# Performance work log

Measured on AMD Instinct MI355X. Metric: run time of the kernel, lower is better.

The kernel has to match this reference:

```python
import jax, jax.numpy as jnp
import numpy as np
import math

N_NODES = 20000
N_EDGES = 320000
DIM = 256
NUM_HEADS = 8


def setup_inputs() -> dict:
    key = jax.random.key(0)
    ks = jax.random.split(key, 8)
    x = jax.random.normal(ks[0], (N_NODES, DIM), dtype=jnp.float32)
    edge_index = jax.random.randint(ks[1], (2, N_EDGES), 0, N_NODES, dtype=jnp.int64)
    edge_attr = jax.random.normal(ks[2], (N_EDGES, DIM), dtype=jnp.float32)
    s = 1.0 / math.sqrt(DIM)
    Wq = jax.random.uniform(ks[3], (DIM, DIM), jnp.float32, -s, s)
    Wk = jax.random.uniform(ks[4], (DIM, DIM), jnp.float32, -s, s)
    Wv = jax.random.uniform(ks[5], (DIM, DIM), jnp.float32, -s, s)
    We = jax.random.uniform(ks[6], (DIM, DIM), jnp.float32, -s, s)
    be = jax.random.uniform(ks[7], (DIM,), jnp.float32, -s, s)
    return {"x": x, "edge_index": edge_index, "edge_attr": edge_attr,
            "Wq": Wq, "Wk": Wk, "Wv": Wv, "We": We, "be": be}


def reference(x, edge_index, edge_attr, Wq, Wk, Wv, We, be):
    N = x.shape[0]
    E = edge_attr.shape[0]
    H = NUM_HEADS
    C = DIM // H  # per-head channels (concat=True)
    src = edge_index[0]  # segment / attention-grouping index
    dst = edge_index[1]
    # Z = edge_attr * x[dst]  -> [E, D]
    Z = edge_attr * x[dst]
    q = x @ Wq.T          # [N, D]
    k = Z @ Wk.T          # [E, D]
    v = Z @ Wv.T          # [E, D]
    edge_out = Z @ We.T + be  # [E, D]
    # split heads
    qh = q.reshape(N, H, C)
    kh = k.reshape(E, H, C)
    vh = v.reshape(E, H, C)
    # per-edge, per-head score: sum(q[src]*k)/sqrt(C)   -> [E, H]
    scores = jnp.einsum('ehc,ehc->eh', qh[src], kh) / math.sqrt(C)
    # segment softmax grouped by src node
    m = jax.ops.segment_max(scores, src, num_segments=N)        # [N, H]
    ex = jnp.exp(scores - m[src])                               # [E, H]
    denom = jax.ops.segment_sum(ex, src, num_segments=N)        # [N, H]
    attn = ex / (denom[src] + 1e-16)                            # [E, H]
    # weighted scatter-sum of values -> [N, H, C] -> [N, D]
    out = jax.ops.segment_sum(attn[:, :, None] * vh, src, num_segments=N)
    out = out.reshape(N, H * C)
    return (out, edge_out)
```

## Files before the change

kernel.cpp:

```cpp
#include <hip/hip_runtime.h>
#include <math.h>

#define NN 20000
#define NE 320000
#define DIM 256

typedef __bf16 bf16x8 __attribute__((ext_vector_type(8)));
typedef float f32x4 __attribute__((ext_vector_type(4)));
typedef int i32x4 __attribute__((ext_vector_type(4)));
typedef unsigned short u16x4 __attribute__((ext_vector_type(4)));

union B8 { i32x4 i; bf16x8 b; };

__device__ __forceinline__ unsigned short f2bf(float f) {
  unsigned int u; __builtin_memcpy(&u, &f, 4);
  u += 0x7fffu + ((u >> 16) & 1u);
  return (unsigned short)(u >> 16);
}
__device__ __forceinline__ float bf2f(unsigned short h) {
  unsigned int u = ((unsigned int)h) << 16;
  float f; __builtin_memcpy(&f, &u, 4);
  return f;
}

#define GLOAD16(gp, lp)                                                        \
  __builtin_amdgcn_global_load_lds(                                            \
      (const __attribute__((address_space(1))) unsigned int*)(gp),             \
      (__attribute__((address_space(3))) unsigned int*)(lp), 16, 0, 0)

__global__ __launch_bounds__(256) void pack_w(const float* __restrict__ W,
                                              unsigned short* __restrict__ wf) {
  int t = blockIdx.x * 256 + threadIdx.x;
  int lane = t & 63, ct = (t >> 6) & 15, ks = t >> 10;
  int col = ct * 16 + (lane & 15);
  int k0 = ks * 32 + (lane >> 4) * 8;
  const float* src = W + col * 256 + k0;
  unsigned int h[8];
#pragma unroll
  for (int j = 0; j < 8; j++) h[j] = f2bf(src[j]);
  i32x4 v;
  v.x = (int)(h[0] | (h[1] << 16));
  v.y = (int)(h[2] | (h[3] << 16));
  v.z = (int)(h[4] | (h[5] << 16));
  v.w = (int)(h[6] | (h[7] << 16));
  ((i32x4*)wf)[t] = v;
}

__global__ __launch_bounds__(256) void zprep(const float* __restrict__ x,
                                             const int* __restrict__ ei,
                                             const float* __restrict__ ea,
                                             unsigned short* __restrict__ zg) {
  int idx = blockIdx.x * 256 + threadIdx.x;
  int lane = idx & 63;
  int bt = (idx >> 6) & 3;
  int ks = (idx >> 8) & 7;
  int tile = idx >> 11;
  int e = tile * 64 + bt * 16 + (lane & 15);
  int kf = ks * 32 + (lane >> 4) * 8;
  int dst = ei[NE + e];
  const f32x4* ap = (const f32x4*)(ea + (size_t)e * DIM + kf);
  const f32x4* xp = (const f32x4*)(x + (size_t)dst * DIM + kf);
  f32x4 p0 = ap[0] * xp[0];
  f32x4 p1 = ap[1] * xp[1];
  unsigned int h[8];
  h[0] = f2bf(p0.x); h[1] = f2bf(p0.y); h[2] = f2bf(p0.z); h[3] = f2bf(p0.w);
  h[4] = f2bf(p1.x); h[5] = f2bf(p1.y); h[6] = f2bf(p1.z); h[7] = f2bf(p1.w);
  i32x4 o;
  o.x = (int)(h[0] | (h[1] << 16));
  o.y = (int)(h[2] | (h[3] << 16));
  o.z = (int)(h[4] | (h[5] << 16));
  o.w = (int)(h[6] | (h[7] << 16));
  size_t byteo = (size_t)tile * 65536 + (size_t)(idx & 2047) * 16;
  *(i32x4*)((char*)zg + byteo) = o;
}

__device__ __forceinline__ void gemm_tile(const unsigned short* zs,
                                          const unsigned short* wf,
                                          int lane, int wv, f32x4 (&acc)[4][4]) {
#pragma unroll 1
  for (int ksI = 0; ksI < 8; ksI++) {
    bf16x8 afr[4], bfr[4];
#pragma unroll
    for (int rt = 0; rt < 4; rt++) {
      int row = rt * 16 + (lane & 15);
      int k = ksI * 32 + (lane >> 4) * 8;
      int byteo = (row * 512 + k * 2) ^ ((row & 7) << 4);
      B8 u; u.i = *(const i32x4*)((const char*)zs + byteo);
      afr[rt] = u.b;
    }
#pragma unroll
    for (int ct = 0; ct < 4; ct++) {
      B8 u; u.i = ((const i32x4*)wf)[ksI * 1024 + (wv * 4 + ct) * 64 + lane];
      bfr[ct] = u.b;
    }
#pragma unroll
    for (int rt = 0; rt < 4; rt++)
#pragma unroll
      for (int ct = 0; ct < 4; ct++)
        acc[rt][ct] = __builtin_amdgcn_mfma_f32_16x16x32_bf16(afr[rt], bfr[ct], acc[rt][ct], 0, 0, 0);
  }
}

__global__ __launch_bounds__(256) void q_kernel(const float* __restrict__ x,
                                                const unsigned short* __restrict__ wf,
                                                float* __restrict__ q) {
  __shared__ unsigned short zs[64 * 256];
  int tid = threadIdx.x, lane = tid & 63, wv = tid >> 6;
  int r0 = blockIdx.x * 64;
  int dcol = lane * 4;
#pragma unroll 4
  for (int rr = 0; rr < 16; rr++) {
    int r = rr * 4 + wv;
    int row = r0 + r;
    f32x4 a = {0.f, 0.f, 0.f, 0.f};
    if (row < NN) a = *(const f32x4*)(x + (size_t)row * DIM + dcol);
    u16x4 z;
    z.x = f2bf(a.x); z.y = f2bf(a.y); z.z = f2bf(a.z); z.w = f2bf(a.w);
    int byteo = (r * 512 + dcol * 2) ^ ((r & 7) << 4);
    *(u16x4*)((char*)zs + byteo) = z;
  }
  __syncthreads();
  f32x4 acc[4][4];
#pragma unroll
  for (int rt = 0; rt < 4; rt++)
#pragma unroll
    for (int ct = 0; ct < 4; ct++) acc[rt][ct] = (f32x4){0.f, 0.f, 0.f, 0.f};
  gemm_tile(zs, wf, lane, wv, acc);
  int cq = lane & 15, rq = lane >> 4;
#pragma unroll
  for (int ct = 0; ct < 4; ct++) {
    int col = wv * 64 + ct * 16 + cq;
#pragma unroll
    for (int rt = 0; rt < 4; rt++) {
#pragma unroll
      for (int j = 0; j < 4; j++) {
        int row = r0 + rt * 16 + rq * 4 + j;
        if (row < NN) q[(size_t)row * DIM + col] = acc[rt][ct][j];
      }
    }
  }
}

__global__ __launch_bounds__(256) void gemm_edge(
    const unsigned short* __restrict__ zg, const int* __restrict__ ei,
    const int* __restrict__ pos,
    const unsigned short* __restrict__ wfk, const unsigned short* __restrict__ wfv,
    const unsigned short* __restrict__ wfe, const float* __restrict__ be,
    const float* __restrict__ q, unsigned short* __restrict__ vws,
    float* __restrict__ sperm, float* __restrict__ edge_out) {
  __shared__ unsigned short zs[64 * 256];
  int tid = threadIdx.x, lane = tid & 63, wv = tid >> 6;
  int rq = lane >> 4, cl = lane & 15;
  int e0 = blockIdx.x * 64;

  int sr4[4], pe4[4];
#pragma unroll
  for (int b = 0; b < 4; b++) {
    sr4[b] = ei[e0 + b * 16 + cl];
    pe4[b] = pos[e0 + b * 16 + cl];
  }

  const unsigned short* wfs[3] = {wfv, wfe, wfk};
  i32x4 wbuf[4][4];
  i32x4 zbuf[2][4];
  f32x4 acc[4][4];

#define LOADW(S, SLOT)                                                         \
  {                                                                            \
    const unsigned short* wfp = wfs[(S) >> 3];                                 \
    _Pragma("unroll") for (int a = 0; a < 4; a++)                              \
        wbuf[SLOT][a] =                                                        \
            ((const i32x4*)wfp)[((S) & 7) * 1024 + (wv * 4 + a) * 64 + lane];  \
  }
#define LOADZ(S, SLOT)                                                         \
  {                                                                            \
    _Pragma("unroll") for (int b = 0; b < 4; b++) {                            \
      int fi = ((S) & 7) * 4 + b;                                              \
      zbuf[SLOT][b] = *(const i32x4*)(zs + fi * 512 + lane * 8);               \
    }                                                                          \
  }
#define GEMM_PASS(P)                                                           \
  _Pragma("unroll") for (int a = 0; a < 4; a++)                                \
      _Pragma("unroll") for (int b = 0; b < 4; b++)                            \
          acc[a][b] = (f32x4){0.f, 0.f, 0.f, 0.f};                             \
  _Pragma("unroll") for (int ks = 0; ks < 8; ks++) {                           \
    const int step = (P) * 8 + ks;                                             \
    if (step + 3 < 24) LOADW(step + 3, (step + 3) & 3);                        \
    if (step + 1 < 24) LOADZ(step + 1, (step + 1) & 1);                        \
    _Pragma("unroll") for (int a = 0; a < 4; a++) {                            \
      B8 w; w.i = wbuf[step & 3][a];                                           \
      _Pragma("unroll") for (int b = 0; b < 4; b++) {                          \
        B8 z; z.i = zbuf[step & 1][b];                                         \
        acc[a][b] = __builtin_amdgcn_mfma_f32_16x16x32_bf16(w.b, z.b,          \
                                                            acc[a][b], 0, 0, 0); \
      }                                                                        \
    }                                                                          \
  }

  {
    const char* gbase = (const char*)zg + (size_t)blockIdx.x * 65536;
#pragma unroll
    for (int s = 0; s < 8; s++) {
      int slab = wv * 8 + s;
      const char* gp = gbase + slab * 1024 + lane * 16;
      unsigned short* lp = zs + slab * 512;
      GLOAD16(gp, lp);
    }
  }
  LOADW(0, 0); LOADW(1, 1); LOADW(2, 2);
  __syncthreads();
  LOADZ(0, 0); LOADZ(1, 1);

  GEMM_PASS(0)
#pragma unroll
  for (int a = 0; a < 4; a++) {
    int ch = wv * 64 + a * 16 + rq * 4;
#pragma unroll
    for (int b = 0; b < 4; b++) {
      int edge = b * 16 + cl;
      u16x4 o;
      o.x = f2bf(acc[a][b][0]); o.y = f2bf(acc[a][b][1]);
      o.z = f2bf(acc[a][b][2]); o.w = f2bf(acc[a][b][3]);
      *(u16x4*)(vws + (size_t)(e0 + edge) * DIM + ch) = o;
    }
  }

  GEMM_PASS(1)
#pragma unroll
  for (int a = 0; a < 4; a++) {
    int ch = wv * 64 + a * 16 + rq * 4;
    f32x4 bias = *(const f32x4*)(be + ch);
#pragma unroll
    for (int b = 0; b < 4; b++) {
      int edge = b * 16 + cl;
      f32x4 o = acc[a][b] + bias;
      *(f32x4*)(edge_out + (size_t)(e0 + edge) * DIM + ch) = o;
    }
  }

  GEMM_PASS(2)
#pragma unroll
  for (int b = 0; b < 4; b++) {
    int edge = b * 16 + cl;
    const float* qp = q + (size_t)sr4[b] * DIM + wv * 64 + rq * 4;
    f32x4 q0 = *(const f32x4*)(qp);
    f32x4 q1 = *(const f32x4*)(qp + 16);
    f32x4 q2 = *(const f32x4*)(qp + 32);
    f32x4 q3 = *(const f32x4*)(qp + 48);
    float s0 = acc[0][b][0] * q0[0] + acc[0][b][1] * q0[1] +
               acc[0][b][2] * q0[2] + acc[0][b][3] * q0[3] +
               acc[1][b][0] * q1[0] + acc[1][b][1] * q1[1] +
               acc[1][b][2] * q1[2] + acc[1][b][3] * q1[3];
    float s1 = acc[2][b][0] * q2[0] + acc[2][b][1] * q2[1] +
               acc[2][b][2] * q2[2] + acc[2][b][3] * q2[3] +
               acc[3][b][0] * q3[0] + acc[3][b][1] * q3[1] +
               acc[3][b][2] * q3[2] + acc[3][b][3] * q3[3];
    s0 += __shfl_xor(s0, 16); s0 += __shfl_xor(s0, 32);
    s1 += __shfl_xor(s1, 16); s1 += __shfl_xor(s1, 32);
    if (lane < 16) {
      sperm[(size_t)pe4[b] * 8 + wv * 2 + 0] = s0 * 0.17677669529663687f;
      sperm[(size_t)pe4[b] * 8 + wv * 2 + 1] = s1 * 0.17677669529663687f;
    }
  }
#undef LOADW
#undef LOADZ
#undef GEMM_PASS
}

__global__ __launch_bounds__(256) void count_kernel(const int* __restrict__ ei,
                                                    int* __restrict__ counts) {
  int e = blockIdx.x * 256 + threadIdx.x;
  if (e < NE) atomicAdd(&counts[ei[e]], 1);
}

__global__ __launch_bounds__(256) void scan_kernel(const int* __restrict__ counts,
                                                   int* __restrict__ offs,
                                                   int* __restrict__ cursor) {
  const int CH = 79;
  int tid = threadIdx.x;
  int lane = tid & 63, wv = tid >> 6;
  int b0 = tid * CH;
  int sum = 0;
  for (int j = 0; j < CH; j++) {
    int i = b0 + j;
    if (i < NN) sum += counts[i];
  }
  int pre = sum;
  for (int d = 1; d < 64; d <<= 1) {
    int t = __shfl_up(pre, d);
    if (lane >= d) pre += t;
  }
  __shared__ int wsum[4];
  if (lane == 63) wsum[wv] = pre;
  __syncthreads();
  int base = 0;
  for (int w = 0; w < wv; w++) base += wsum[w];
  int running = base + pre - sum;
  for (int j = 0; j < CH; j++) {
    int i = b0 + j;
    if (i < NN) {
      offs[i] = running;
      cursor[i] = running;
      running += counts[i];
    }
  }
  if (tid == 255) offs[NN] = running;
}

__global__ __launch_bounds__(256) void fill_kernel(const int* __restrict__ ei,
                                                   int* __restrict__ cursor,
                                                   int* __restrict__ eids,
                                                   int* __restrict__ pos) {
  int e = blockIdx.x * 256 + threadIdx.x;
  if (e < NE) {
    int p = atomicAdd(&cursor[ei[e]], 1);
    eids[p] = e;
    pos[e] = p;
  }
}

__global__ __launch_bounds__(256) void node_kernel(const int* __restrict__ offs,
                                                   const int* __restrict__ eids,
                                                   const float* __restrict__ sperm,
                                                   const unsigned short* __restrict__ vws,
                                                   float* __restrict__ out) {
  int tid = threadIdx.x;
  int n = blockIdx.x * 4 + (tid >> 6);
  int lane = tid & 63, h = lane >> 3;
  int o0 = offs[n], deg = offs[n + 1] - o0;
  float m = -INFINITY, s = 0.f;
  float a0 = 0.f, a1 = 0.f, a2 = 0.f, a3 = 0.f;
  int e = (deg > 0) ? eids[o0] : 0;
  u16x4 v = *(const u16x4*)(vws + (size_t)e * DIM + lane * 4);
  for (int i = 0; i < deg; i++) {
    int en = (i + 1 < deg) ? eids[o0 + i + 1] : e;
    u16x4 vn = *(const u16x4*)(vws + (size_t)en * DIM + lane * 4);
    float sc = sperm[(size_t)(o0 + i) * 8 + h];
    float mn = fmaxf(m, sc);
    float scale = __expf(m - mn);
    float p = __expf(sc - mn);
    s = s * scale + p;
    m = mn;
    a0 = a0 * scale + p * bf2f(v.x);
    a1 = a1 * scale + p * bf2f(v.y);
    a2 = a2 * scale + p * bf2f(v.z);
    a3 = a3 * scale + p * bf2f(v.w);
    v = vn;
  }
  float inv = 1.f / (s + 1e-16f);
  f32x4 o;
  o.x = a0 * inv; o.y = a1 * inv; o.z = a2 * inv; o.w = a3 * inv;
  *(f32x4*)(out + (size_t)n * DIM + lane * 4) = o;
}

extern "C" void kernel_launch(void* const* d_in, const int* in_sizes, int n_in,
                              void* d_out, int out_size, void* d_ws, size_t ws_size,
                              hipStream_t stream) {
  const float* x = (const float*)d_in[0];
  const int* ei = (const int*)d_in[1];
  const float* ea = (const float*)d_in[2];
  const float* Wq = (const float*)d_in[3];
  const float* Wk = (const float*)d_in[4];
  const float* Wv = (const float*)d_in[5];
  const float* We = (const float*)d_in[6];
  const float* be = (const float*)d_in[7];

  float* out = (float*)d_out;
  float* edge_out = out + (size_t)NN * DIM;
  unsigned short* zg = (unsigned short*)edge_out;
  float* q = out;

  char* ws = (char*)d_ws;
  unsigned short* wfq = (unsigned short*)(ws + 0);
  unsigned short* wfk = (unsigned short*)(ws + 131072);
  unsigned short* wfv = (unsigned short*)(ws + 262144);
  unsigned short* wfe = (unsigned short*)(ws + 393216);
  unsigned short* vws = (unsigned short*)(ws + 524288);
  float* sperm = (float*)(ws + 524288 + 163840000);
  int* counts = (int*)(ws + 524288 + 163840000 + 10240000);
  int* offs   = (int*)(ws + 524288 + 163840000 + 10240000 + 80000);
  int* cursor = (int*)(ws + 524288 + 163840000 + 10240000 + 160016);
  int* eids   = (int*)(ws + 524288 + 163840000 + 10240000 + 240016);
  int* pos    = (int*)(ws + 524288 + 163840000 + 10240000 + 240016 + 1280000);

  hipMemsetAsync(counts, 0, NN * sizeof(int), stream);

  pack_w<<<32, 256, 0, stream>>>(Wq, wfq);
  pack_w<<<32, 256, 0, stream>>>(Wk, wfk);
  pack_w<<<32, 256, 0, stream>>>(Wv, wfv);
  pack_w<<<32, 256, 0, stream>>>(We, wfe);

  zprep<<<NE * 32 / 256, 256, 0, stream>>>(x, ei, ea, zg);

  count_kernel<<<(NE + 255) / 256, 256, 0, stream>>>(ei, counts);
  scan_kernel<<<1, 256, 0, stream>>>(counts, offs, cursor);
  fill_kernel<<<(NE + 255) / 256, 256, 0, stream>>>(ei, cursor, eids, pos);

  q_kernel<<<(NN + 63) / 64, 256, 0, stream>>>(x, wfq, q);

  gemm_edge<<<NE / 64, 256, 0, stream>>>(zg, ei, pos, wfk, wfv, wfe, be, q,
                                         vws, sperm, edge_out);

  node_kernel<<<NN / 4, 256, 0, stream>>>(offs, eids, sperm, vws, out);
}
```

Baseline: 620.9 us.

## Restage zprep through LDS and split edge GEMM across eight waves

zprep now has each thread read contiguous 64-byte spans of edge_attr and x, stages the bf16 results in shared memory, then writes the MFMA-fragment layout with coalesced 32-byte stores. gemm_edge moves to 512 threads with each wave covering 32 output channels instead of 64. It drops the LDS staging of Z and loads Z fragments straight from global memory, and reorders the passes to V, K, E. This lowers register pressure and raises occupancy, at the cost of each wave re-reading the Z tile from global/L2 and thinner double-buffered prefetching.

```diff
diff --git a/kernel.cpp b/kernel.cpp
--- a/kernel.cpp
+++ b/kernel.cpp
@@ -22,11 +22,6 @@
   float f; __builtin_memcpy(&f, &u, 4);
   return f;
 }
-
-#define GLOAD16(gp, lp)                                                        \
-  __builtin_amdgcn_global_load_lds(                                            \
-      (const __attribute__((address_space(1))) unsigned int*)(gp),             \
-      (__attribute__((address_space(3))) unsigned int*)(lp), 16, 0, 0)
 
 __global__ __launch_bounds__(256) void pack_w(const float* __restrict__ W,
                                               unsigned short* __restrict__ wf) {
@@ -50,28 +45,38 @@
                                              const int* __restrict__ ei,
                                              const float* __restrict__ ea,
                                              unsigned short* __restrict__ zg) {
-  int idx = blockIdx.x * 256 + threadIdx.x;
-  int lane = idx & 63;
-  int bt = (idx >> 6) & 3;
-  int ks = (idx >> 8) & 7;
-  int tile = idx >> 11;
-  int e = tile * 64 + bt * 16 + (lane & 15);
-  int kf = ks * 32 + (lane >> 4) * 8;
+  __shared__ char lds[8192];
+  int tid = threadIdx.x;
+  int blk = blockIdx.x;
+  int er = tid >> 4, kc = tid & 15;
+  int e = blk * 16 + er;
   int dst = ei[NE + e];
-  const f32x4* ap = (const f32x4*)(ea + (size_t)e * DIM + kf);
-  const f32x4* xp = (const f32x4*)(x + (size_t)dst * DIM + kf);
-  f32x4 p0 = ap[0] * xp[0];
-  f32x4 p1 = ap[1] * xp[1];
-  unsigned int h[8];
-  h[0] = f2bf(p0.x); h[1] = f2bf(p0.y); h[2] = f2bf(p0.z); h[3] = f2bf(p0.w);
-  h[4] = f2bf(p1.x); h[5] = f2bf(p1.y); h[6] = f2bf(p1.z); h[7] = f2bf(p1.w);
-  i32x4 o;
-  o.x = (int)(h[0] | (h[1] << 16));
-  o.y = (int)(h[2] | (h[3] << 16));
-  o.z = (int)(h[4] | (h[5] << 16));
-  o.w = (int)(h[6] | (h[7] << 16));
-  size_t byteo = (size_t)tile * 65536 + (size_t)(idx & 2047) * 16;
-  *(i32x4*)((char*)zg + byteo) = o;
+  const f32x4* ap = (const f32x4*)(ea + (size_t)e * DIM + kc * 16);
+  const f32x4* xp = (const f32x4*)(x + (size_t)dst * DIM + kc * 16);
+  int ks = kc >> 1, rqb = (kc & 1) * 2;
+#pragma unroll
+  for (int j = 0; j < 2; j++) {
+    f32x4 p0 = ap[j * 2 + 0] * xp[j * 2 + 0];
+    f32x4 p1 = ap[j * 2 + 1] * xp[j * 2 + 1];
+    unsigned int h[8];
+    h[0] = f2bf(p0.x); h[1] = f2bf(p0.y); h[2] = f2bf(p0.z); h[3] = f2bf(p0.w);
+    h[4] = f2bf(p1.x); h[5] = f2bf(p1.y); h[6] = f2bf(p1.z); h[7] = f2bf(p1.w);
+    i32x4 o;
+    o.x = (int)(h[0] | (h[1] << 16));
+    o.y = (int)(h[2] | (h[3] << 16));
+    o.z = (int)(h[4] | (h[5] << 16));
+    o.w = (int)(h[6] | (h[7] << 16));
+    *(i32x4*)(lds + ks * 1024 + (rqb + j) * 256 + er * 16) = o;
+  }
+  __syncthreads();
+  int ks_o = tid >> 5, m = tid & 31;
+  int bt = blk & 3;
+  char* outp = (char*)zg + (size_t)(blk >> 2) * 65536 +
+               (size_t)(ks_o * 4 + bt) * 1024 + m * 32;
+  i32x4 v0 = *(i32x4*)(lds + tid * 32);
+  i32x4 v1 = *(i32x4*)(lds + tid * 32 + 16);
+  *(i32x4*)outp = v0;
+  *(i32x4*)(outp + 16) = v1;
 }
 
 __device__ __forceinline__ void gemm_tile(const unsigned short* zs,
@@ -141,17 +146,17 @@
   }
 }
 
-__global__ __launch_bounds__(256) void gemm_edge(
+__global__ __launch_bounds__(512) void gemm_edge(
     const unsigned short* __restrict__ zg, const int* __restrict__ ei,
     const int* __restrict__ pos,
     const unsigned short* __restrict__ wfk, const unsigned short* __restrict__ wfv,
     const unsigned short* __restrict__ wfe, const float* __restrict__ be,
     const float* __restrict__ q, unsigned short* __restrict__ vws,
     float* __restrict__ sperm, float* __restrict__ edge_out) {
-  __shared__ unsigned short zs[64 * 256];
   int tid = threadIdx.x, lane = tid & 63, wv = tid >> 6;
   int rq = lane >> 4, cl = lane & 15;
   int e0 = blockIdx.x * 64;
+  const i32x4* gz = (const i32x4*)((const char*)zg + (size_t)blockIdx.x * 65536);
 
   int sr4[4], pe4[4];
 #pragma unroll
@@ -160,35 +165,33 @@
     pe4[b] = pos[e0 + b * 16 + cl];
   }
 
-  const unsigned short* wfs[3] = {wfv, wfe, wfk};
-  i32x4 wbuf[4][4];
+  const unsigned short* wfs[3] = {wfv, wfk, wfe};
+  i32x4 wbuf[2][2];
   i32x4 zbuf[2][4];
-  f32x4 acc[4][4];
+  f32x4 acc[2][4];
 
 #define LOADW(S, SLOT)                                                         \
   {                                                                            \
     const unsigned short* wfp = wfs[(S) >> 3];                                 \
-    _Pragma("unroll") for (int a = 0; a < 4; a++)                              \
+    _Pragma("unroll") for (int a = 0; a < 2; a++)                              \
         wbuf[SLOT][a] =                                                        \
-            ((const i32x4*)wfp)[((S) & 7) * 1024 + (wv * 4 + a) * 64 + lane];  \
+            ((const i32x4*)wfp)[((S) & 7) * 1024 + (wv * 2 + a) * 64 + lane];  \
   }
 #define LOADZ(S, SLOT)                                                         \
   {                                                                            \
-    _Pragma("unroll") for (int b = 0; b < 4; b++) {                            \
-      int fi = ((S) & 7) * 4 + b;                                              \
-      zbuf[SLOT][b] = *(const i32x4*)(zs + fi * 512 + lane * 8);               \
-    }                                                                          \
+    _Pragma("unroll") for (int b = 0; b < 4; b++)                              \
+      zbuf[SLOT][b] = gz[(((S) & 7) * 4 + b) * 64 + lane];                     \
   }
 #define GEMM_PASS(P)                                                           \
-  _Pragma("unroll") for (int a = 0; a < 4; a++)                                \
+  _Pragma("unroll") for (int a = 0; a < 2; a++)                                \
       _Pragma("unroll") for (int b = 0; b < 4; b++)                            \
           acc[a][b] = (f32x4){0.f, 0.f, 0.f, 0.f};                             \
   _Pragma("unroll") for (int ks = 0; ks < 8; ks++) {                           \
     const int step = (P) * 8 + ks;                                             \
-    if (step + 3 < 24) LOADW(step + 3, (step + 3) & 3);                        \
-    if (step + 1 < 24) LOADZ(step + 1, (step + 1) & 1);                        \
-    _Pragma("unroll") for (int a = 0; a < 4; a++) {                            \
-      B8 w; w.i = wbuf[step & 3][a];                                           \
+    if (step + 1 < 24) { LOADW(step + 1, (step + 1) & 1);                      \
+                         LOADZ(step + 1, (step + 1) & 1); }                    \
+    _Pragma("unroll") for (int a = 0; a < 2; a++) {                            \
+      B8 w; w.i = wbuf[step & 1][a];                                           \
       _Pragma("unroll") for (int b = 0; b < 4; b++) {                          \
         B8 z; z.i = zbuf[step & 1][b];                                         \
         acc[a][b] = __builtin_amdgcn_mfma_f32_16x16x32_bf16(w.b, z.b,          \
@@ -197,24 +200,12 @@
     }                                                                          \
   }
 
-  {
-    const char* gbase = (const char*)zg + (size_t)blockIdx.x * 65536;
-#pragma unroll
-    for (int s = 0; s < 8; s++) {
-      int slab = wv * 8 + s;
-      const char* gp = gbase + slab * 1024 + lane * 16;
-      unsigned short* lp = zs + slab * 512;
-      GLOAD16(gp, lp);
-    }
-  }
-  LOADW(0, 0); LOADW(1, 1); LOADW(2, 2);
-  __syncthreads();
-  LOADZ(0, 0); LOADZ(1, 1);
+  LOADW(0, 0); LOADZ(0, 0);
 
   GEMM_PASS(0)
 #pragma unroll
-  for (int a = 0; a < 4; a++) {
-    int ch = wv * 64 + a * 16 + rq * 4;
+  for (int a = 0; a < 2; a++) {
+    int ch = wv * 32 + a * 16 + rq * 4;
 #pragma unroll
     for (int b = 0; b < 4; b++) {
       int edge = b * 16 + cl;
@@ -227,39 +218,32 @@
 
   GEMM_PASS(1)
 #pragma unroll
-  for (int a = 0; a < 4; a++) {
-    int ch = wv * 64 + a * 16 + rq * 4;
+  for (int b = 0; b < 4; b++) {
+    const float* qp = q + (size_t)sr4[b] * DIM + wv * 32 + rq * 4;
+    f32x4 q0 = *(const f32x4*)(qp);
+    f32x4 q1 = *(const f32x4*)(qp + 16);
+    float s = acc[0][b][0] * q0[0] + acc[0][b][1] * q0[1] +
+              acc[0][b][2] * q0[2] + acc[0][b][3] * q0[3] +
+              acc[1][b][0] * q1[0] + acc[1][b][1] * q1[1] +
+              acc[1][b][2] * q1[2] + acc[1][b][3] * q1[3];
+    s += __shfl_xor(s, 16);
+    s += __shfl_xor(s, 32);
+    if (lane < 16) {
+      sperm[(size_t)pe4[b] * 8 + wv] = s * 0.17677669529663687f;
+    }
+  }
+
+  GEMM_PASS(2)
+  __syncthreads();
+#pragma unroll
+  for (int a = 0; a < 2; a++) {
+    int ch = wv * 32 + a * 16 + rq * 4;
     f32x4 bias = *(const f32x4*)(be + ch);
 #pragma unroll
     for (int b = 0; b < 4; b++) {
       int edge = b * 16 + cl;
       f32x4 o = acc[a][b] + bias;
       *(f32x4*)(edge_out + (size_t)(e0 + edge) * DIM + ch) = o;
-    }
-  }
-
-  GEMM_PASS(2)
-#pragma unroll
-  for (int b = 0; b < 4; b++) {
-    int edge = b * 16 + cl;
-    const float* qp = q + (size_t)sr4[b] * DIM + wv * 64 + rq * 4;
-    f32x4 q0 = *(const f32x4*)(qp);
-    f32x4 q1 = *(const f32x4*)(qp + 16);
-    f32x4 q2 = *(const f32x4*)(qp + 32);
-    f32x4 q3 = *(const f32x4*)(qp + 48);
-    float s0 = acc[0][b][0] * q0[0] + acc[0][b][1] * q0[1] +
-               acc[0][b][2] * q0[2] + acc[0][b][3] * q0[3] +
-               acc[1][b][0] * q1[0] + acc[1][b][1] * q1[1] +
-               acc[1][b][2] * q1[2] + acc[1][b][3] * q1[3];
-    float s1 = acc[2][b][0] * q2[0] + acc[2][b][1] * q2[1] +
-               acc[2][b][2] * q2[2] + acc[2][b][3] * q2[3] +
-               acc[3][b][0] * q3[0] + acc[3][b][1] * q3[1] +
-               acc[3][b][2] * q3[2] + acc[3][b][3] * q3[3];
-    s0 += __shfl_xor(s0, 16); s0 += __shfl_xor(s0, 32);
-    s1 += __shfl_xor(s1, 16); s1 += __shfl_xor(s1, 32);
-    if (lane < 16) {
-      sperm[(size_t)pe4[b] * 8 + wv * 2 + 0] = s0 * 0.17677669529663687f;
-      sperm[(size_t)pe4[b] * 8 + wv * 2 + 1] = s1 * 0.17677669529663687f;
     }
   }
 #undef LOADW
@@ -390,7 +374,7 @@
   pack_w<<<32, 256, 0, stream>>>(Wv, wfv);
   pack_w<<<32, 256, 0, stream>>>(We, wfe);
 
-  zprep<<<NE * 32 / 256, 256, 0, stream>>>(x, ei, ea, zg);
+  zprep<<<NE / 16, 256, 0, stream>>>(x, ei, ea, zg);
 
   count_kernel<<<(NE + 255) / 256, 256, 0, stream>>>(ei, counts);
   scan_kernel<<<1, 256, 0, stream>>>(counts, offs, cursor);
@@ -398,7 +382,7 @@
 
   q_kernel<<<(NN + 63) / 64, 256, 0, stream>>>(x, wfq, q);
 
-  gemm_edge<<<NE / 64, 256, 0, stream>>>(zg, ei, pos, wfk, wfv, wfe, be, q,
+  gemm_edge<<<NE / 64, 512, 0, stream>>>(zg, ei, pos, wfk, wfv, wfe, be, q,
                                          vws, sperm, edge_out);
 
   node_kernel<<<NN / 4, 256, 0, stream>>>(offs, eids, sperm, vws, out);
```

New measurement: 662.5 us. 6.7% more time.
